# Kernel tuning notes

Hardware: AMD Instinct MI355X
Metric: run time of the kernel (lower is better)

## Reference

```python
import jax, jax.numpy as jnp
import numpy as np

SEQ, BATCH, D, N = 256, 4, 512, 32768
TEMP = 0.5


def setup_inputs() -> dict:
    key = jax.random.key(0)
    ks = jax.random.split(key, 16)
    d = D
    # xavier_uniform with gain 1/sqrt(2) for square [d,d]: limit = gain*sqrt(6/(d+d))
    lim_t = (1.0 / np.sqrt(2.0)) * np.sqrt(6.0 / (d + d))
    lim_g1 = np.sqrt(6.0 / (2 * d + d))  # default kaiming-ish scale approximated by xavier
    lim_g2 = np.sqrt(6.0 / (d + 1))
    inp = {
        "q": jax.random.normal(ks[0], (SEQ, BATCH, D), dtype=jnp.float32),
        "prev_layer_output": jax.random.normal(ks[1], (SEQ, BATCH, D), dtype=jnp.float32),
        "Wq": jax.random.uniform(ks[2], (D, D), jnp.float32, -lim_t, lim_t),
        "bq": jnp.zeros((D,), jnp.float32),
        "Wk": jax.random.uniform(ks[3], (D, D), jnp.float32, -lim_t, lim_t),
        "bk": jnp.zeros((D,), jnp.float32),
        "Wv": jax.random.uniform(ks[4], (D, D), jnp.float32, -lim_t, lim_t),
        "bv": jnp.zeros((D,), jnp.float32),
        "Wg1": jax.random.uniform(ks[5], (D, 2 * D), jnp.float32, -lim_g1, lim_g1),
        "bg1": jnp.zeros((D,), jnp.float32),
        "Wg2": jax.random.uniform(ks[6], (1, D), jnp.float32, -lim_g2, lim_g2),
        "bg2": jnp.zeros((1,), jnp.float32),
        "dstore_k": jax.random.normal(ks[7], (N, D), dtype=jnp.float32),
        "dstore_v": jax.random.normal(ks[8], (N, D), dtype=jnp.float32),
    }
    return inp


def reference(q, prev_layer_output, Wq, bq, Wk, bk, Wv, bv, Wg1, bg1, Wg2, bg2, dstore_k, dstore_v):
    # [S,B,D] -> [B,S,D]
    qb = jnp.transpose(q, (1, 0, 2))
    prevb = jnp.transpose(prev_layer_output, (1, 0, 2))
    # enable_tune projections
    _q = qb @ Wq.T + bq                      # [B,S,D]
    _k = dstore_k @ Wk.T + bk                # [N,D]
    _v = dstore_v @ Wv.T + bv                # [N,D]
    _q = _q * (D ** -0.5)
    # attention over datastore, temperature-scaled softmax
    logits = jnp.einsum("bsd,nd->bsn", _q, _k) / TEMP  # [B,S,N]
    w = jax.nn.softmax(logits, axis=-1)
    attn = jnp.einsum("bsn,nd->bsd", w, _v)            # [B,S,D]
    # gated residual fusion
    cat = jnp.concatenate([attn, prevb], axis=-1)      # [B,S,2D]
    h = jax.nn.relu(cat @ Wg1.T + bg1)                 # [B,S,D]
    sigma = jax.nn.sigmoid(h @ Wg2.T + bg2)            # [B,S,1]
    res = attn * sigma + prevb * (1.0 - sigma)
    return jnp.transpose(res, (1, 0, 2))               # [S,B,D]
```

## Files before the change

kernel.cpp:

```cpp
#include <hip/hip_runtime.h>
#include <hip/hip_bf16.h>
#include <cstdint>
#include <cstddef>


typedef unsigned short u16;
typedef u16    u16x8 __attribute__((ext_vector_type(8)));
typedef u16    u16x4 __attribute__((ext_vector_type(4)));
typedef __bf16 bf16x8 __attribute__((ext_vector_type(8)));
typedef float  f32x4 __attribute__((ext_vector_type(4)));

#define MFMA16(a, b, c) __builtin_amdgcn_mfma_f32_16x16x32_bf16( \
    __builtin_bit_cast(bf16x8, (a)), __builtin_bit_cast(bf16x8, (b)), (c), 0, 0, 0)

__device__ __forceinline__ u16 f2bf(float f) {
  unsigned u = __builtin_bit_cast(unsigned, f);
  u += 0x7fffu + ((u >> 16) & 1u);
  return (u16)(u >> 16);
}

__device__ __forceinline__ void glds16(const u16* g, u16* l) {
  __builtin_amdgcn_global_load_lds(
      (const __attribute__((address_space(1))) unsigned*)g,
      (__attribute__((address_space(3))) unsigned*)l, 16, 0, 0);
}

__global__ __launch_bounds__(256) void prep_kfrag(const float* __restrict__ src,
                                                  u16* __restrict__ dst) {
  const int sub = blockIdx.x;
  const int t = threadIdx.x;
  const float* s0 = src + (size_t)sub * 32 * 512;
  u16* d0 = dst + (size_t)sub * 16384;
#pragma unroll
  for (int u = 0; u < 8; u++) {
    int ci = t + 256 * u;
    int nh = ci >> 10, ks = (ci >> 6) & 15, ln = ci & 63;
    int qd = ln >> 4, l15 = ln & 15;
    const float* sp = s0 + (size_t)(nh * 16 + l15) * 512 + ks * 32 + qd * 8;
    float4 a = *(const float4*)sp;
    float4 b = *(const float4*)(sp + 4);
    u16x8 o = {f2bf(a.x), f2bf(a.y), f2bf(a.z), f2bf(a.w),
               f2bf(b.x), f2bf(b.y), f2bf(b.z), f2bf(b.w)};
    *(u16x8*)(d0 + (size_t)ci * 8) = o;
  }
}

__global__ __launch_bounds__(256) void prep_vt(const float* __restrict__ v,
                                               u16* __restrict__ vt) {
  __shared__ u16 Lt[64 * 72];
  const int n0 = blockIdx.x * 64, d0 = blockIdx.y * 64;
  const int t = threadIdx.x;
  const int n = t >> 2, c4 = t & 3;
#pragma unroll
  for (int i = 0; i < 4; i++) {
    int col = (c4 + 4 * i) * 4;
    float4 x = *(const float4*)(v + (size_t)(n0 + n) * 512 + d0 + col);
    Lt[(col + 0) * 72 + n] = f2bf(x.x);
    Lt[(col + 1) * 72 + n] = f2bf(x.y);
    Lt[(col + 2) * 72 + n] = f2bf(x.z);
    Lt[(col + 3) * 72 + n] = f2bf(x.w);
  }
  __syncthreads();
#pragma unroll
  for (int u = 0; u < 2; u++) {
    int unit = t + 256 * u;
    int d = unit >> 3, un = unit & 7;
    *(u16x8*)(vt + (size_t)(d0 + d) * 32768 + n0 + un * 8) =
        *(const u16x8*)&Lt[d * 72 + un * 8];
  }
}

template <bool TRANSB, bool CONCAT, bool RELU, bool OUTBF16, bool ROWSCALE>
__global__ __launch_bounds__(256, 2) void gemm64(
    const float* __restrict__ A, const float* __restrict__ A2,
    const float* __restrict__ B, const float* __restrict__ bias,
    const float* __restrict__ lvec, float alpha, void* __restrict__ Cv,
    int M, int N, int K) {
  __shared__ u16 As[64 * 72];
  __shared__ u16 Bs[64 * 72];
  const int tid = threadIdx.x;
  const int w = tid >> 6, lane = tid & 63, quad = lane >> 4, l15 = lane & 15;
  const int m0 = blockIdx.y * 64, n0 = blockIdx.x * 64;
  const int arow = tid >> 2, ac4 = tid & 3;
  float rs = 1.0f;
  if (ROWSCALE) rs = 1.0f / lvec[m0 + arow];
  const f32x4 fzero = {0.f, 0.f, 0.f, 0.f};
  f32x4 acc[4];
#pragma unroll
  for (int i = 0; i < 4; i++) acc[i] = fzero;

  for (int k0 = 0; k0 < K; k0 += 64) {
    __syncthreads();
    {
      const float* src;
      if (CONCAT)
        src = (k0 < 512) ? (A + (size_t)(m0 + arow) * 512 + k0)
                         : (A2 + (size_t)(m0 + arow) * 512 + (k0 - 512));
      else
        src = A + (size_t)(m0 + arow) * K + k0;
#pragma unroll
      for (int i = 0; i < 4; i++) {
        int col = (ac4 + 4 * i) * 4;
        float4 x = *(const float4*)(src + col);
        if (ROWSCALE) { x.x *= rs; x.y *= rs; x.z *= rs; x.w *= rs; }
        u16x4 o = {f2bf(x.x), f2bf(x.y), f2bf(x.z), f2bf(x.w)};
        *(u16x4*)&As[arow * 72 + col] = o;
      }
    }
    if (TRANSB) {
      const float* src = B + (size_t)(n0 + arow) * K + k0;
#pragma unroll
      for (int i = 0; i < 4; i++) {
        int col = (ac4 + 4 * i) * 4;
        float4 x = *(const float4*)(src + col);
        u16x4 o = {f2bf(x.x), f2bf(x.y), f2bf(x.z), f2bf(x.w)};
        *(u16x4*)&Bs[arow * 72 + col] = o;
      }
    } else {
      const float* src = B + (size_t)(k0 + arow) * N + n0;
#pragma unroll
      for (int i = 0; i < 4; i++) {
        int col = (ac4 + 4 * i) * 4;
        float4 x = *(const float4*)(src + col);
        Bs[(col + 0) * 72 + arow] = f2bf(x.x);
        Bs[(col + 1) * 72 + arow] = f2bf(x.y);
        Bs[(col + 2) * 72 + arow] = f2bf(x.z);
        Bs[(col + 3) * 72 + arow] = f2bf(x.w);
      }
    }
    __syncthreads();
#pragma unroll
    for (int ks = 0; ks < 2; ks++) {
      u16x8 af = *(const u16x8*)&As[(w * 16 + l15) * 72 + ks * 32 + quad * 8];
#pragma unroll
      for (int nt = 0; nt < 4; nt++) {
        u16x8 bf = *(const u16x8*)&Bs[(nt * 16 + l15) * 72 + ks * 32 + quad * 8];
        acc[nt] = MFMA16(af, bf, acc[nt]);
      }
    }
  }
#pragma unroll
  for (int nt = 0; nt < 4; nt++) {
    int col = n0 + nt * 16 + l15;
    float b = bias ? bias[col] : 0.f;
#pragma unroll
    for (int i = 0; i < 4; i++) {
      int row = m0 + w * 16 + quad * 4 + i;
      float y = (acc[nt][i] + b) * alpha;
      if (RELU) y = fmaxf(y, 0.f);
      if (OUTBF16)
        ((u16*)Cv)[(size_t)row * N + col] = f2bf(y);
      else
        ((float*)Cv)[(size_t)row * N + col] = y;
    }
  }
}

__global__ void cq_kernel(const float* __restrict__ q1,
                          const float* __restrict__ bk,
                          float* __restrict__ cq) {
  int r = blockIdx.x, lane = threadIdx.x;
  float s = 0.f;
#pragma unroll
  for (int k = 0; k < 512; k += 64) s += q1[(size_t)r * 512 + k + lane] * bk[k + lane];
#pragma unroll
  for (int off = 32; off; off >>= 1) s += __shfl_down(s, off, 64);
  if (lane == 0) cq[r] = 2.0f * s;
}

__global__ __launch_bounds__(512, 2) void flash(
    const u16* __restrict__ kfr,
    const u16* __restrict__ vt,
    const u16* __restrict__ q2,
    const float* __restrict__ cq,
    float* __restrict__ racc,
    float* __restrict__ lacc) {
  __shared__ __align__(16) u16 Kb[2][16384];
  __shared__ __align__(16) u16 Es[2][64 * 40];
  const int tid = threadIdx.x;
  const int w = tid >> 6, lane = tid & 63, quad = lane >> 4, l15 = lane & 15;
  const int x = blockIdx.x & 7, j = blockIdx.x >> 3;
  const int ch = 2 * x + (j & 1), qt = j >> 1;
  const int qbase = qt * 64;
  const int qg = w >> 1, nh = w & 1;
  const int colb = w * 64;

  u16x8 qf[16];
  {
    const u16* qp = q2 + (size_t)(qbase + qg * 16 + l15) * 512 + quad * 8;
#pragma unroll
    for (int ks = 0; ks < 16; ks++) qf[ks] = *(const u16x8*)(qp + ks * 32);
  }
  float cq4[4];
#pragma unroll
  for (int i = 0; i < 4; i++) cq4[i] = cq[qbase + qg * 16 + quad * 4 + i];
  float lp[4] = {0.f, 0.f, 0.f, 0.f};
  const f32x4 fzero = {0.f, 0.f, 0.f, 0.f};
  f32x4 acc[4][4];
#pragma unroll
  for (int a = 0; a < 4; a++)
#pragma unroll
    for (int b = 0; b < 4; b++) acc[a][b] = fzero;

  const u16* kg0 = kfr + (size_t)(ch * 64) * 16384 + w * 2048 + lane * 8;
  const u16* vp0 = vt + (size_t)(colb + l15) * 32768 + ch * 2048 + quad * 8;

  u16x8 bvA[4], bvB[4];

#define GLDS_K(SUB, BI)                                                  \
  {                                                                      \
    const u16* gb = kg0 + (size_t)(SUB) * 16384;                         \
    _Pragma("unroll") for (int u = 0; u < 4; u++)                        \
        glds16(gb + u * 512, &Kb[BI][w * 2048 + u * 512]);               \
  }
#define LOAD_V(BV, SUB)                                                  \
  {                                                                      \
    _Pragma("unroll") for (int ct = 0; ct < 4; ct++)                     \
        BV[ct] = *(const u16x8*)(vp0 + (size_t)ct * (16 * 32768) +       \
                                 (SUB) * 32);                            \
  }
#define LOGITS(BI, SV)                                                   \
  {                                                                      \
    f32x4 s0_ = fzero, s1_ = fzero;                                      \
    const u16* kb_ = &Kb[BI][nh * 8192 + lane * 8];                      \
    _Pragma("unroll") for (int ks = 0; ks < 16; ks += 2) {               \
      u16x8 k0_ = *(const u16x8*)(kb_ + ks * 512);                       \
      u16x8 k1_ = *(const u16x8*)(kb_ + (ks + 1) * 512);                 \
      s0_ = MFMA16(qf[ks], k0_, s0_);                                    \
      s1_ = MFMA16(qf[ks + 1], k1_, s1_);                                \
    }                                                                    \
    SV = s0_ + s1_;                                                      \
  }
#define PV_STEP(ER, BV)                                                  \
  {                                                                      \
    u16x8 ef[4];                                                         \
    _Pragma("unroll") for (int q2i = 0; q2i < 4; q2i++)                  \
      ef[q2i] = *(const u16x8*)&(ER)[(q2i * 16 + l15) * 40 + quad * 8];  \
    _Pragma("unroll") for (int ct = 0; ct < 4; ct++)                     \
      _Pragma("unroll") for (int q2i = 0; q2i < 4; q2i++)                \
        acc[q2i][ct] = MFMA16(ef[q2i], BV[ct], acc[q2i][ct]);            \
  }
#define EXPW(EW, SV)                                                     \
  {                                                                      \
    _Pragma("unroll") for (int i = 0; i < 4; i++) {                      \
      float e = __expf(SV[i] + cq4[i]);                                  \
      lp[i] += e;                                                        \
      (EW)[(qg * 16 + quad * 4 + i) * 40 + nh * 16 + l15] = f2bf(e);     \
    }                                                                    \
  }
#define WAIT_BAR(VN)                                                     \
  {                                                                      \
    asm volatile("s_waitcnt vmcnt(" #VN ") lgkmcnt(0)" ::: "memory");    \
    __builtin_amdgcn_s_barrier();                                        \
    __builtin_amdgcn_sched_barrier(0);                                   \
  }

  GLDS_K(0, 0);
  GLDS_K(1, 1);
  LOAD_V(bvA, 0);
  asm volatile("s_waitcnt vmcnt(8)" ::: "memory");
  __builtin_amdgcn_s_barrier();
  __builtin_amdgcn_sched_barrier(0);
  {
    f32x4 s;
    LOGITS(0, s);
    EXPW(Es[0], s);
  }

#pragma unroll 1
  for (int sb = 1; sb < 62; sb += 2) {
    WAIT_BAR(0);
    GLDS_K(sb + 1, 0);
    LOAD_V(bvB, sb);
    __builtin_amdgcn_sched_barrier(0);
    __builtin_amdgcn_s_setprio(1);
    f32x4 s;
    PV_STEP(Es[0], bvA);
    LOGITS(1, s);
    __builtin_amdgcn_s_setprio(0);
    EXPW(Es[1], s);
    WAIT_BAR(0);
    GLDS_K(sb + 2, 1);
    LOAD_V(bvA, sb + 1);
    __builtin_amdgcn_sched_barrier(0);
    __builtin_amdgcn_s_setprio(1);
    f32x4 t;
    PV_STEP(Es[1], bvB);
    LOGITS(0, t);
    __builtin_amdgcn_s_setprio(0);
    EXPW(Es[0], t);
  }

  WAIT_BAR(0);
  LOAD_V(bvB, 63);
  __builtin_amdgcn_sched_barrier(0);
  {
    __builtin_amdgcn_s_setprio(1);
    f32x4 s;
    PV_STEP(Es[0], bvA);
    LOGITS(1, s);
    __builtin_amdgcn_s_setprio(0);
    EXPW(Es[1], s);
  }
  WAIT_BAR(0);
  PV_STEP(Es[1], bvB);

#undef GLDS_K
#undef LOAD_V
#undef LOGITS
#undef PV_STEP
#undef EXPW
#undef WAIT_BAR

#pragma unroll
  for (int q2i = 0; q2i < 4; q2i++)
#pragma unroll
    for (int ct = 0; ct < 4; ct++) {
      int col = colb + ct * 16 + l15;
#pragma unroll
      for (int i = 0; i < 4; i++) {
        int row = qbase + q2i * 16 + quad * 4 + i;
        atomicAdd(&racc[(size_t)row * 512 + col], acc[q2i][ct][i]);
      }
    }
#pragma unroll
  for (int i = 0; i < 4; i++) {
    float v = lp[i];
#pragma unroll
    for (int off = 1; off < 16; off <<= 1) v += __shfl_xor(v, off, 64);
    if (l15 == 0) atomicAdd(&lacc[qbase + qg * 16 + quad * 4 + i], v);
  }
}

__global__ __launch_bounds__(256) void finalize(
    const float* __restrict__ h, const float* __restrict__ attn,
    const float* __restrict__ prev, const float* __restrict__ wg2,
    const float* __restrict__ bg2, float* __restrict__ out) {
  __shared__ float red[4];
  int r = blockIdx.x, t = threadIdx.x;
  const float* hr = h + (size_t)r * 512;
  float p = hr[t] * wg2[t] + hr[t + 256] * wg2[t + 256];
#pragma unroll
  for (int off = 32; off; off >>= 1) p += __shfl_down(p, off, 64);
  if ((t & 63) == 0) red[t >> 6] = p;
  __syncthreads();
  float dot = red[0] + red[1] + red[2] + red[3];
  float sg = 1.f / (1.f + __expf(-(dot + bg2[0])));
  size_t base = (size_t)r * 512;
  out[base + t] = attn[base + t] * sg + prev[base + t] * (1.f - sg);
  out[base + t + 256] = attn[base + t + 256] * sg + prev[base + t + 256] * (1.f - sg);
}

extern "C" void kernel_launch(void* const* d_in, const int* in_sizes, int n_in,
                              void* d_out, int out_size, void* d_ws, size_t ws_size,
                              hipStream_t stream) {
  const float* q    = (const float*)d_in[0];
  const float* prev = (const float*)d_in[1];
  const float* Wq   = (const float*)d_in[2];
  const float* bq   = (const float*)d_in[3];
  const float* Wk   = (const float*)d_in[4];
  const float* bk   = (const float*)d_in[5];
  const float* Wv   = (const float*)d_in[6];
  const float* bv   = (const float*)d_in[7];
  const float* Wg1  = (const float*)d_in[8];
  const float* bg1  = (const float*)d_in[9];
  const float* Wg2  = (const float*)d_in[10];
  const float* bg2  = (const float*)d_in[11];
  const float* dk   = (const float*)d_in[12];
  const float* dv   = (const float*)d_in[13];
  float* out = (float*)d_out;

  char* ws = (char*)d_ws;
  u16*   kfr  = (u16*)(ws);
  u16*   vt   = (u16*)(ws + 33554432);
  float* racc = (float*)(ws + 67108864);
  float* lacc = (float*)(ws + 69206016);
  float* cqv  = (float*)(ws + 69210112);
  u16*   q2   = (u16*)(ws + 69214208);
  float* q1   = (float*)(ws + 70262784);
  float* attn = (float*)(ws + 72359936);
  float* h    = q1;

  prep_kfrag<<<1024, 256, 0, stream>>>(dk, kfr);
  prep_vt<<<dim3(512, 8), 256, 0, stream>>>(dv, vt);
  gemm64<true, false, false, false, false><<<dim3(8, 16), 256, 0, stream>>>(
      q, nullptr, Wq, bq, nullptr, 0.044194173824159216f, q1, 1024, 512, 512);
  cq_kernel<<<1024, 64, 0, stream>>>(q1, bk, cqv);
  gemm64<false, false, false, true, false><<<dim3(8, 16), 256, 0, stream>>>(
      q1, nullptr, Wk, nullptr, nullptr, 2.0f, q2, 1024, 512, 512);
  hipMemsetAsync(racc, 0, 2097152 + 4096, stream);
  flash<<<256, 512, 0, stream>>>(kfr, vt, q2, cqv, racc, lacc);
  gemm64<true, false, false, false, true><<<dim3(8, 16), 256, 0, stream>>>(
      racc, nullptr, Wv, bv, lacc, 1.0f, attn, 1024, 512, 512);
  gemm64<true, true, true, false, false><<<dim3(8, 16), 256, 0, stream>>>(
      attn, prev, Wg1, bg1, nullptr, 1.0f, h, 1024, 512, 1024);
  finalize<<<1024, 256, 0, stream>>>(h, attn, prev, Wg2, bg2, out);
}
```

Baseline: 430.3 us.

## Deepen K prefetch pipeline to four LDS stages in flash kernel

Grows the LDS buffer for K tiles from two to four stages and restructures the main loop into a software pipeline that keeps K tiles about three steps ahead. Waits become partial (vmcnt 12) instead of draining all loads at each barrier. V register double buffering now uses an indexed array, and the loop is unrolled by four to rotate buffer indices. The aim is to hide global-memory latency better. In exchange, LDS use per block roughly doubles, which likely stops two blocks from fitting on one CU and lowers occupancy.

After: 419.4 us. 2.5% less time.

```diff
diff --git a/kernel.cpp b/kernel.cpp
--- a/kernel.cpp
+++ b/kernel.cpp
@@ -175,7 +175,7 @@
     const float* __restrict__ cq,
     float* __restrict__ racc,
     float* __restrict__ lacc) {
-  __shared__ __align__(16) u16 Kb[2][16384];
+  __shared__ __align__(16) u16 Kb[4][16384];
   __shared__ __align__(16) u16 Es[2][64 * 40];
   const int tid = threadIdx.x;
   const int w = tid >> 6, lane = tid & 63, quad = lane >> 4, l15 = lane & 15;
@@ -205,7 +205,7 @@
   const u16* kg0 = kfr + (size_t)(ch * 64) * 16384 + w * 2048 + lane * 8;
   const u16* vp0 = vt + (size_t)(colb + l15) * 32768 + ch * 2048 + quad * 8;
 
-  u16x8 bvA[4], bvB[4];
+  u16x8 bvv[2][4];
 
 #define GLDS_K(SUB, BI)                                                  \
   {                                                                      \
@@ -213,11 +213,11 @@
     _Pragma("unroll") for (int u = 0; u < 4; u++)                        \
         glds16(gb + u * 512, &Kb[BI][w * 2048 + u * 512]);               \
   }
-#define LOAD_V(BV, SUB)                                                  \
+#define LOAD_V(BP, SUB)                                                  \
   {                                                                      \
     _Pragma("unroll") for (int ct = 0; ct < 4; ct++)                     \
-        BV[ct] = *(const u16x8*)(vp0 + (size_t)ct * (16 * 32768) +       \
-                                 (SUB) * 32);                            \
+        bvv[BP][ct] = *(const u16x8*)(vp0 + (size_t)ct * (16 * 32768) +  \
+                                      (SUB) * 32);                       \
   }
 #define LOGITS(BI, SV)                                                   \
   {                                                                      \
@@ -231,14 +231,14 @@
     }                                                                    \
     SV = s0_ + s1_;                                                      \
   }
-#define PV_STEP(ER, BV)                                                  \
+#define PV_STEP(ER, BP)                                                  \
   {                                                                      \
     u16x8 ef[4];                                                         \
     _Pragma("unroll") for (int q2i = 0; q2i < 4; q2i++)                  \
       ef[q2i] = *(const u16x8*)&(ER)[(q2i * 16 + l15) * 40 + quad * 8];  \
     _Pragma("unroll") for (int ct = 0; ct < 4; ct++)                     \
       _Pragma("unroll") for (int q2i = 0; q2i < 4; q2i++)                \
-        acc[q2i][ct] = MFMA16(ef[q2i], BV[ct], acc[q2i][ct]);            \
+        acc[q2i][ct] = MFMA16(ef[q2i], bvv[BP][ct], acc[q2i][ct]);       \
   }
 #define EXPW(EW, SV)                                                     \
   {                                                                      \
@@ -248,69 +248,81 @@
       (EW)[(qg * 16 + quad * 4 + i) * 40 + nh * 16 + l15] = f2bf(e);     \
     }                                                                    \
   }
-#define WAIT_BAR(VN)                                                     \
-  {                                                                      \
-    asm volatile("s_waitcnt vmcnt(" #VN ") lgkmcnt(0)" ::: "memory");    \
+#define WB(N)                                                            \
+  {                                                                      \
+    asm volatile("s_waitcnt vmcnt(" #N ") lgkmcnt(0)" ::: "memory");     \
     __builtin_amdgcn_s_barrier();                                        \
     __builtin_amdgcn_sched_barrier(0);                                   \
   }
+#define REGION(S, P)                                                     \
+  {                                                                      \
+    WB(12);                                                              \
+    LOAD_V((P) & 1, (S));                                                \
+    GLDS_K((S) + 3, ((P) + 3) & 3);                                      \
+    __builtin_amdgcn_sched_barrier(0);                                   \
+    __builtin_amdgcn_s_setprio(1);                                       \
+    f32x4 sv_;                                                           \
+    PV_STEP(Es[((P) + 1) & 1], ((P) + 1) & 1);                           \
+    LOGITS((P) & 3, sv_);                                                \
+    __builtin_amdgcn_s_setprio(0);                                       \
+    EXPW(Es[(P) & 1], sv_);                                              \
+  }
+#define REGION_NOK(S, P)                                                 \
+  {                                                                      \
+    WB(12);                                                              \
+    LOAD_V((P) & 1, (S));                                                \
+    __builtin_amdgcn_sched_barrier(0);                                   \
+    __builtin_amdgcn_s_setprio(1);                                       \
+    f32x4 sv_;                                                           \
+    PV_STEP(Es[((P) + 1) & 1], ((P) + 1) & 1);                           \
+    LOGITS((P) & 3, sv_);                                                \
+    __builtin_amdgcn_s_setprio(0);                                       \
+    EXPW(Es[(P) & 1], sv_);                                              \
+  }
 
   GLDS_K(0, 0);
   GLDS_K(1, 1);
-  LOAD_V(bvA, 0);
+  GLDS_K(2, 2);
   asm volatile("s_waitcnt vmcnt(8)" ::: "memory");
   __builtin_amdgcn_s_barrier();
   __builtin_amdgcn_sched_barrier(0);
+
   {
-    f32x4 s;
-    LOGITS(0, s);
-    EXPW(Es[0], s);
-  }
-
-#pragma unroll 1
-  for (int sb = 1; sb < 62; sb += 2) {
-    WAIT_BAR(0);
-    GLDS_K(sb + 1, 0);
-    LOAD_V(bvB, sb);
+    LOAD_V(0, 0);
+    GLDS_K(3, 3);
     __builtin_amdgcn_sched_barrier(0);
     __builtin_amdgcn_s_setprio(1);
-    f32x4 s;
-    PV_STEP(Es[0], bvA);
-    LOGITS(1, s);
+    f32x4 sv_;
+    LOGITS(0, sv_);
     __builtin_amdgcn_s_setprio(0);
-    EXPW(Es[1], s);
-    WAIT_BAR(0);
-    GLDS_K(sb + 2, 1);
-    LOAD_V(bvA, sb + 1);
-    __builtin_amdgcn_sched_barrier(0);
-    __builtin_amdgcn_s_setprio(1);
-    f32x4 t;
-    PV_STEP(Es[1], bvB);
-    LOGITS(0, t);
-    __builtin_amdgcn_s_setprio(0);
-    EXPW(Es[0], t);
-  }
-
-  WAIT_BAR(0);
-  LOAD_V(bvB, 63);
-  __builtin_amdgcn_sched_barrier(0);
-  {
-    __builtin_amdgcn_s_setprio(1);
-    f32x4 s;
-    PV_STEP(Es[0], bvA);
-    LOGITS(1, s);
-    __builtin_amdgcn_s_setprio(0);
-    EXPW(Es[1], s);
-  }
-  WAIT_BAR(0);
-  PV_STEP(Es[1], bvB);
+    EXPW(Es[0], sv_);
+  }
+  REGION(1, 1);
+
+#pragma unroll 1
+  for (int s0 = 2; s0 < 58; s0 += 4) {
+    REGION(s0 + 0, 2);
+    REGION(s0 + 1, 3);
+    REGION(s0 + 2, 0);
+    REGION(s0 + 3, 1);
+  }
+  REGION(58, 2);
+  REGION(59, 3);
+  REGION(60, 0);
+  REGION_NOK(61, 1);
+  REGION_NOK(62, 2);
+  REGION_NOK(63, 3);
+  WB(0);
+  PV_STEP(Es[1], 1);
 
 #undef GLDS_K
 #undef LOAD_V
 #undef LOGITS
 #undef PV_STEP
 #undef EXPW
-#undef WAIT_BAR
+#undef WB
+#undef REGION
+#undef REGION_NOK
 
 #pragma unroll
   for (int q2i = 0; q2i < 4; q2i++)
```
